# Kernel optimization log

Hardware: AMD Instinct MI355X
Metric: run time of the kernel (lower is better)

The kernel has to match this reference:

```python
import jax, jax.numpy as jnp
import numpy as np

EPS = 1e-5
NUM_GROUPS = 8


def setup_inputs() -> dict:
    key = jax.random.key(0)
    ks = jax.random.split(key, 7)
    B, C, D, H, W = 2, 128, 16, 16, 16
    s = 1.0 / np.sqrt(C)
    return {
        "x": jax.random.normal(ks[0], (B, C, D, H, W), dtype=jnp.float32),
        "Wq": jax.random.normal(ks[1], (C, C), dtype=jnp.float32) * s,
        "Wk": jax.random.normal(ks[2], (C, C), dtype=jnp.float32) * s,
        "Wv": jax.random.normal(ks[3], (C, C), dtype=jnp.float32) * s,
        "Wo": jax.random.normal(ks[4], (C, C), dtype=jnp.float32) * s,
        "gamma": jnp.ones((C,), dtype=jnp.float32),
        "beta": jnp.zeros((C,), dtype=jnp.float32),
    }


def reference(x, Wq, Wk, Wv, Wo, gamma, beta):
    B, C = x.shape[0], x.shape[1]
    spatial = x.shape[2:]
    xf = x.reshape(B, C, -1)  # [B, C, N]

    # 1x1 conv == channel-mixing matmul
    q = jnp.einsum('oc,bcn->bon', Wq, xf)
    k = jnp.einsum('oc,bcn->bon', Wk, xf)
    v = jnp.einsum('oc,bcn->bon', Wv, xf)

    # unscaled attention: qk[b,n,m] = sum_c q[b,c,n] k[b,c,m]
    w = jax.nn.softmax(jnp.einsum('bcn,bcm->bnm', q, k), axis=-1)  # [B, N, N]
    # h = v @ w^T : h[b,c,n] = sum_m v[b,c,m] w[b,n,m]
    h = jnp.einsum('bcm,bnm->bcn', v, w)
    h = jnp.einsum('oc,bcn->bon', Wo, h)

    y = xf + h
    # GroupNorm(8, C) over (C//G, N) per group
    g = y.reshape(B, NUM_GROUPS, C // NUM_GROUPS, -1)
    mu = jnp.mean(g, axis=(2, 3), keepdims=True)
    var = jnp.mean(jnp.square(g - mu), axis=(2, 3), keepdims=True)
    gn = ((g - mu) * jax.lax.rsqrt(var + EPS)).reshape(B, C, -1)
    out = gn * gamma[None, :, None] + beta[None, :, None]
    out = out * jax.nn.sigmoid(out)  # SiLU
    return out.reshape(B, C, *spatial)
```

## Files before the change

### kernel.cpp

```cpp
#include <hip/hip_runtime.h>

#define CC 128
#define NN 4096
#define NB 2
#define NSPLIT 8
#define TK 64
#define ITERS 8

typedef unsigned short ushort;
typedef unsigned int uint;
typedef __attribute__((ext_vector_type(8))) _Float16 h8;
typedef __attribute__((ext_vector_type(8))) short s8;
typedef __attribute__((ext_vector_type(4))) float f4;
#define MFMA16(a, b, c) __builtin_amdgcn_mfma_f32_16x16x32_f16(a, b, c, 0, 0, 0)
#define MFMAB(a, b, c)  __builtin_amdgcn_mfma_f32_16x16x32_bf16(a, b, c, 0, 0, 0)

__device__ __forceinline__ ushort f2h(float f) {
  _Float16 h = (_Float16)f;
  return *(ushort*)&h;
}
__device__ __forceinline__ ushort f2bf(float f) {
  uint u = __float_as_uint(f);
  u += 0x7fffu + ((u >> 16) & 1u);
  return (ushort)(u >> 16);
}
__device__ __forceinline__ float bf2f(ushort u) {
  return __uint_as_float((uint)u << 16);
}

__global__ __launch_bounds__(256) void qkv_mm(
    const float* __restrict__ x, const float* __restrict__ Wq,
    const float* __restrict__ Wk, const float* __restrict__ Wv,
    ushort* __restrict__ qT, ushort* __restrict__ kT, ushort* __restrict__ vB,
    float* __restrict__ stats) {
  __shared__ ushort Wh[CC][136];
  __shared__ ushort xs[32][136];
  const int t = threadIdx.x;
  const int n0 = blockIdx.x * 32;
  const int b = blockIdx.y;
  const int which = blockIdx.z;

  if (blockIdx.x == 0 && b == 0 && which == 0 && t < 32) stats[t] = 0.f;

  {
    int c0 = (t & 31) * 4;
    int n4 = (t >> 5) * 4;
    float4 r0 = *(const float4*)&x[((size_t)b * CC + c0 + 0) * NN + n0 + n4];
    float4 r1 = *(const float4*)&x[((size_t)b * CC + c0 + 1) * NN + n0 + n4];
    float4 r2 = *(const float4*)&x[((size_t)b * CC + c0 + 2) * NN + n0 + n4];
    float4 r3 = *(const float4*)&x[((size_t)b * CC + c0 + 3) * NN + n0 + n4];
    ushort4 w0, w1, w2, w3;
    w0.x = f2h(r0.x); w0.y = f2h(r1.x); w0.z = f2h(r2.x); w0.w = f2h(r3.x);
    w1.x = f2h(r0.y); w1.y = f2h(r1.y); w1.z = f2h(r2.y); w1.w = f2h(r3.y);
    w2.x = f2h(r0.z); w2.y = f2h(r1.z); w2.z = f2h(r2.z); w2.w = f2h(r3.z);
    w3.x = f2h(r0.w); w3.y = f2h(r1.w); w3.z = f2h(r2.w); w3.w = f2h(r3.w);
    *(ushort4*)&xs[n4 + 0][c0] = w0;
    *(ushort4*)&xs[n4 + 1][c0] = w1;
    *(ushort4*)&xs[n4 + 2][c0] = w2;
    *(ushort4*)&xs[n4 + 3][c0] = w3;
  }

  {
    const float* W = (which == 0) ? Wq : (which == 1) ? Wk : Wv;
#pragma unroll
    for (int i = 0; i < 16; ++i) {
      int slot = t + 256 * i;
      int o = slot >> 5, c4 = (slot & 31) * 4;
      float4 w4 = *(const float4*)&W[o * CC + c4];
      ushort4 p; p.x = f2h(w4.x); p.y = f2h(w4.y); p.z = f2h(w4.z); p.w = f2h(w4.w);
      *(ushort4*)&Wh[o][c4] = p;
    }
  }
  __syncthreads();

  const int wv = t >> 6, lane = t & 63;
  const int quad = lane >> 4, l16 = lane & 15;

  if (which < 2) {
    ushort* out = which ? kT : qT;
    f4 acc[2][2];
#pragma unroll
    for (int ot = 0; ot < 2; ++ot)
#pragma unroll
      for (int nt = 0; nt < 2; ++nt) acc[ot][nt] = (f4){0.f, 0.f, 0.f, 0.f};
#pragma unroll
    for (int kk = 0; kk < 4; ++kk) {
      h8 a0 = *(const h8*)&Wh[(wv * 2 + 0) * 16 + l16][kk * 32 + quad * 8];
      h8 a1 = *(const h8*)&Wh[(wv * 2 + 1) * 16 + l16][kk * 32 + quad * 8];
#pragma unroll
      for (int nt = 0; nt < 2; ++nt) {
        h8 bb = *(const h8*)&xs[nt * 16 + l16][kk * 32 + quad * 8];
        acc[0][nt] = MFMA16(a0, bb, acc[0][nt]);
        acc[1][nt] = MFMA16(a1, bb, acc[1][nt]);
      }
    }
#pragma unroll
    for (int ot = 0; ot < 2; ++ot)
#pragma unroll
      for (int nt = 0; nt < 2; ++nt) {
        f4 a = acc[ot][nt];
        ushort4 p; p.x = f2h(a[0]); p.y = f2h(a[1]); p.z = f2h(a[2]); p.w = f2h(a[3]);
        *(ushort4*)&out[((size_t)b * NN + n0 + nt * 16 + l16) * CC +
                        (wv * 2 + ot) * 16 + quad * 4] = p;
      }
  } else {
    f4 acc[2][2];
#pragma unroll
    for (int ci = 0; ci < 2; ++ci)
#pragma unroll
      for (int nt = 0; nt < 2; ++nt) acc[ci][nt] = (f4){0.f, 0.f, 0.f, 0.f};
#pragma unroll
    for (int kk = 0; kk < 4; ++kk) {
      h8 a0 = *(const h8*)&xs[0 * 16 + l16][kk * 32 + quad * 8];
      h8 a1 = *(const h8*)&xs[1 * 16 + l16][kk * 32 + quad * 8];
      h8 b0 = *(const h8*)&Wh[(wv * 2 + 0) * 16 + l16][kk * 32 + quad * 8];
      h8 b1 = *(const h8*)&Wh[(wv * 2 + 1) * 16 + l16][kk * 32 + quad * 8];
      acc[0][0] = MFMA16(a0, b0, acc[0][0]);
      acc[0][1] = MFMA16(a1, b0, acc[0][1]);
      acc[1][0] = MFMA16(a0, b1, acc[1][0]);
      acc[1][1] = MFMA16(a1, b1, acc[1][1]);
    }
#pragma unroll
    for (int ci = 0; ci < 2; ++ci)
#pragma unroll
      for (int nt = 0; nt < 2; ++nt) {
        f4 a = acc[ci][nt];
        ushort4 p; p.x = f2bf(a[0]); p.y = f2bf(a[1]); p.z = f2bf(a[2]); p.w = f2bf(a[3]);
        *(ushort4*)&vB[((size_t)b * CC + (wv * 2 + ci) * 16 + l16) * NN +
                       n0 + nt * 16 + quad * 4] = p;
      }
  }
}

__global__ __launch_bounds__(256) void attn_split(
    const ushort* __restrict__ qTg, const ushort* __restrict__ kTg,
    const ushort* __restrict__ vBg, ushort* __restrict__ Op,
    float* __restrict__ Lg) {
  __shared__ ushort ksT[TK][136];
  __shared__ ushort vs[CC][72];
  __shared__ ushort psb[4][32][72];

  const int t = threadIdx.x;
  const int b = blockIdx.z;
  const int split = blockIdx.y;
  const int n0 = blockIdx.x * 128;
  const int wv = t >> 6;
  const int lane = t & 63;
  const int quad = lane >> 4;
  const int l16 = lane & 15;
  const int nw = n0 + wv * 32;
  const int m00 = split * (NN / NSPLIT);

  const int krow = t >> 4, kcol = (t & 15) * 8;
  const int vrow = t >> 3, vcol = (t & 7) * 8;
  const ushort* kbp = kTg + ((size_t)b * NN + m00 + krow) * CC + kcol;
  const ushort* vbp = vBg + ((size_t)b * CC + vrow) * NN + m00 + vcol;

  const size_t qb0 = ((size_t)b * NN + nw + l16) * CC + quad * 8;
  const size_t qb1 = qb0 + (size_t)16 * CC;
  h8 aq[2][4];
#pragma unroll
  for (int kk = 0; kk < 4; ++kk) {
    aq[0][kk] = *(const h8*)&qTg[qb0 + kk * 32];
    aq[1][kk] = *(const h8*)&qTg[qb1 + kk * 32];
  }

  int4 k0 = *(const int4*)&kbp[0];
  int4 k1 = *(const int4*)&kbp[16 * CC];
  int4 k2 = *(const int4*)&kbp[32 * CC];
  int4 k3 = *(const int4*)&kbp[48 * CC];
  int4 v0 = *(const int4*)&vbp[0];
  int4 v1 = *(const int4*)&vbp[(size_t)32 * NN];
  int4 v2 = *(const int4*)&vbp[(size_t)64 * NN];
  int4 v3 = *(const int4*)&vbp[(size_t)96 * NN];

  s8 ones;
#pragma unroll
  for (int i = 0; i < 8; ++i) ones[i] = (short)0x3F80;

  f4 o[2][8];
#pragma unroll
  for (int j = 0; j < 2; ++j)
#pragma unroll
    for (int ct = 0; ct < 8; ++ct) o[j][ct] = (f4){0.f, 0.f, 0.f, 0.f};
  f4 oL[2];
  oL[0] = (f4){0.f, 0.f, 0.f, 0.f};
  oL[1] = (f4){0.f, 0.f, 0.f, 0.f};

  for (int kt = 0; kt < ITERS; ++kt) {
    *(int4*)&ksT[krow][kcol]      = k0;
    *(int4*)&ksT[krow + 16][kcol] = k1;
    *(int4*)&ksT[krow + 32][kcol] = k2;
    *(int4*)&ksT[krow + 48][kcol] = k3;
    *(int4*)&vs[vrow][vcol]       = v0;
    *(int4*)&vs[vrow + 32][vcol]  = v1;
    *(int4*)&vs[vrow + 64][vcol]  = v2;
    *(int4*)&vs[vrow + 96][vcol]  = v3;
    __syncthreads();

    {
      int ktn = (kt + 1 < ITERS) ? kt + 1 : kt;
      const ushort* kp = kbp + (size_t)ktn * TK * CC;
      const ushort* vp = vbp + (size_t)ktn * TK;
      k0 = *(const int4*)&kp[0];
      k1 = *(const int4*)&kp[16 * CC];
      k2 = *(const int4*)&kp[32 * CC];
      k3 = *(const int4*)&kp[48 * CC];
      v0 = *(const int4*)&vp[0];
      v1 = *(const int4*)&vp[(size_t)32 * NN];
      v2 = *(const int4*)&vp[(size_t)64 * NN];
      v3 = *(const int4*)&vp[(size_t)96 * NN];
    }

    f4 s[2][4];
#pragma unroll
    for (int j = 0; j < 2; ++j)
#pragma unroll
      for (int mt = 0; mt < 4; ++mt) s[j][mt] = (f4){0.f, 0.f, 0.f, 0.f};
#pragma unroll
    for (int kk = 0; kk < 4; ++kk) {
      h8 b0 = *(const h8*)&ksT[ 0 + l16][kk * 32 + quad * 8];
      h8 b1 = *(const h8*)&ksT[16 + l16][kk * 32 + quad * 8];
      h8 b2 = *(const h8*)&ksT[32 + l16][kk * 32 + quad * 8];
      h8 b3 = *(const h8*)&ksT[48 + l16][kk * 32 + quad * 8];
#pragma unroll
      for (int j = 0; j < 2; ++j) {
        s[j][0] = MFMA16(b0, aq[j][kk], s[j][0]);
        s[j][1] = MFMA16(b1, aq[j][kk], s[j][1]);
        s[j][2] = MFMA16(b2, aq[j][kk], s[j][2]);
        s[j][3] = MFMA16(b3, aq[j][kk], s[j][3]);
      }
    }

#pragma unroll
    for (int j = 0; j < 2; ++j)
#pragma unroll
      for (int mt = 0; mt < 4; ++mt) {
        ushort4 pk;
        pk.x = f2bf(__expf(s[j][mt][0]));
        pk.y = f2bf(__expf(s[j][mt][1]));
        pk.z = f2bf(__expf(s[j][mt][2]));
        pk.w = f2bf(__expf(s[j][mt][3]));
        *(ushort4*)&psb[wv][j * 16 + l16][mt * 16 + quad * 4] = pk;
      }

#pragma unroll
    for (int mk = 0; mk < 2; ++mk) {
      s8 bp0 = *(const s8*)&psb[wv][ 0 + l16][mk * 32 + quad * 8];
      s8 bp1 = *(const s8*)&psb[wv][16 + l16][mk * 32 + quad * 8];
#pragma unroll
      for (int ct = 0; ct < 8; ++ct) {
        s8 a = *(const s8*)&vs[ct * 16 + l16][mk * 32 + quad * 8];
        o[0][ct] = MFMAB(a, bp0, o[0][ct]);
        o[1][ct] = MFMAB(a, bp1, o[1][ct]);
      }
      oL[0] = MFMAB(ones, bp0, oL[0]);
      oL[1] = MFMAB(ones, bp1, oL[1]);
    }
    __syncthreads();
  }

#pragma unroll
  for (int j = 0; j < 2; ++j) {
    if (quad == 0)
      Lg[((size_t)(split * NB + b)) * NN + nw + j * 16 + l16] = oL[j][0];
    size_t nb_ = ((size_t)(split * NB + b) * NN + nw + j * 16 + l16) * CC + quad * 4;
    ushort4 p;
#pragma unroll
    for (int ct = 0; ct < 8; ++ct) {
      f4 a = o[j][ct];
      p.x = f2bf(a[0]); p.y = f2bf(a[1]); p.z = f2bf(a[2]); p.w = f2bf(a[3]);
      *(ushort4*)&Op[nb_ + ct * 16] = p;
    }
  }
}

__global__ __launch_bounds__(256) void proj_mm(
    const float* __restrict__ x, const float* __restrict__ Wo,
    const ushort* __restrict__ Op, const float* __restrict__ Lg,
    float* __restrict__ y, float* __restrict__ stats) {
  __shared__ ushort Wh[CC][136];
  __shared__ ushort hT[32][136];
  __shared__ float Linv[32];
  const int t = threadIdx.x;
  const int n0 = blockIdx.x * 32;
  const int b = blockIdx.y;

#pragma unroll
  for (int i = 0; i < 16; ++i) {
    int slot = t + 256 * i;
    int o = slot >> 5, c4 = (slot & 31) * 4;
    float4 w4 = *(const float4*)&Wo[o * CC + c4];
    ushort4 p; p.x = f2h(w4.x); p.y = f2h(w4.y); p.z = f2h(w4.z); p.w = f2h(w4.w);
    *(ushort4*)&Wh[o][c4] = p;
  }
  if (t < 32) {
    float l = 0.f;
#pragma unroll
    for (int s = 0; s < NSPLIT; ++s)
      l += Lg[(size_t)(s * NB + b) * NN + n0 + t];
    Linv[t] = 1.f / l;
  }
  __syncthreads();

#pragma unroll
  for (int i = 0; i < 16; ++i) {
    int slot = t + 256 * i;
    int n = slot >> 5, c4 = (slot & 31) * 4;
    size_t base = ((size_t)(n0 + n)) * CC + c4;
    float a0 = 0.f, a1 = 0.f, a2 = 0.f, a3 = 0.f;
#pragma unroll
    for (int s = 0; s < NSPLIT; ++s) {
      ushort4 u = *(const ushort4*)&Op[(size_t)(s * NB + b) * NN * CC + base];
      a0 += bf2f(u.x); a1 += bf2f(u.y); a2 += bf2f(u.z); a3 += bf2f(u.w);
    }
    float li = Linv[n];
    ushort4 p;
    p.x = f2h(a0 * li); p.y = f2h(a1 * li);
    p.z = f2h(a2 * li); p.w = f2h(a3 * li);
    *(ushort4*)&hT[n][c4] = p;
  }
  __syncthreads();

  const int wv = t >> 6, lane = t & 63;
  const int quad = lane >> 4, l16 = lane & 15;

  f4 acc[2][2];
#pragma unroll
  for (int nt = 0; nt < 2; ++nt)
#pragma unroll
    for (int ot = 0; ot < 2; ++ot) acc[nt][ot] = (f4){0.f, 0.f, 0.f, 0.f};
#pragma unroll
  for (int kk = 0; kk < 4; ++kk) {
    h8 a0 = *(const h8*)&hT[0 * 16 + l16][kk * 32 + quad * 8];
    h8 a1 = *(const h8*)&hT[1 * 16 + l16][kk * 32 + quad * 8];
    h8 b0 = *(const h8*)&Wh[(wv * 2 + 0) * 16 + l16][kk * 32 + quad * 8];
    h8 b1 = *(const h8*)&Wh[(wv * 2 + 1) * 16 + l16][kk * 32 + quad * 8];
    acc[0][0] = MFMA16(a0, b0, acc[0][0]);
    acc[0][1] = MFMA16(a0, b1, acc[0][1]);
    acc[1][0] = MFMA16(a1, b0, acc[1][0]);
    acc[1][1] = MFMA16(a1, b1, acc[1][1]);
  }

#pragma unroll
  for (int ot = 0; ot < 2; ++ot) {
    const int o = (wv * 2 + ot) * 16 + l16;
    const int g = wv * 2 + ot;
    float s = 0.f, sq = 0.f;
#pragma unroll
    for (int nt = 0; nt < 2; ++nt) {
      size_t addr = ((size_t)b * CC + o) * NN + n0 + nt * 16 + quad * 4;
      float4 xv = *(const float4*)&x[addr];
      f4 a = acc[nt][ot];
      float4 yy;
      yy.x = a[0] + xv.x; yy.y = a[1] + xv.y;
      yy.z = a[2] + xv.z; yy.w = a[3] + xv.w;
      *(float4*)&y[addr] = yy;
      s += yy.x + yy.y + yy.z + yy.w;
      sq += yy.x * yy.x + yy.y * yy.y + yy.z * yy.z + yy.w * yy.w;
    }
#pragma unroll
    for (int off = 1; off < 64; off <<= 1) {
      s += __shfl_xor(s, off);
      sq += __shfl_xor(sq, off);
    }
    if (lane == 0) {
      atomicAdd(&stats[(b * 8 + g) * 2 + 0], s);
      atomicAdd(&stats[(b * 8 + g) * 2 + 1], sq);
    }
  }
}

__global__ __launch_bounds__(256) void gn_silu(
    const float* __restrict__ y, const float* __restrict__ stats,
    const float* __restrict__ gamma, const float* __restrict__ beta,
    float* __restrict__ out) {
  const int tid = blockIdx.x * 256 + threadIdx.x;
  const int i4 = tid * 4;
  const int c = (i4 >> 12) & (CC - 1);
  const int b = i4 >> 19;
  const int g = c >> 4;
  const float inv = 1.f / 65536.f;
  float sum = stats[(b * 8 + g) * 2 + 0];
  float sq  = stats[(b * 8 + g) * 2 + 1];
  float mean = sum * inv;
  float var = sq * inv - mean * mean;
  float rs = rsqrtf(var + 1e-5f);
  float ga = gamma[c], be = beta[c];
  float4 v4 = *(const float4*)&y[i4];
  float4 r;
  float o;
  o = (v4.x - mean) * rs * ga + be; r.x = o / (1.f + __expf(-o));
  o = (v4.y - mean) * rs * ga + be; r.y = o / (1.f + __expf(-o));
  o = (v4.z - mean) * rs * ga + be; r.z = o / (1.f + __expf(-o));
  o = (v4.w - mean) * rs * ga + be; r.w = o / (1.f + __expf(-o));
  *(float4*)&out[i4] = r;
}

extern "C" void kernel_launch(void* const* d_in, const int* in_sizes, int n_in,
                              void* d_out, int out_size, void* d_ws, size_t ws_size,
                              hipStream_t stream) {
  const float* x     = (const float*)d_in[0];
  const float* Wq    = (const float*)d_in[1];
  const float* Wk    = (const float*)d_in[2];
  const float* Wv    = (const float*)d_in[3];
  const float* Wo    = (const float*)d_in[4];
  const float* gamma = (const float*)d_in[5];
  const float* beta  = (const float*)d_in[6];
  float* out = (float*)d_out;
  float* ws  = (float*)d_ws;

  const size_t M = (size_t)NB * CC * NN;
  ushort* Op = (ushort*)ws;
  ushort* qT = (ushort*)ws + (size_t)NSPLIT * M;
  ushort* kT = qT + M;
  ushort* vB = kT + M;
  float* y = (float*)(vB + M);
  float* Lg = y + M;
  float* stats = Lg + (size_t)NSPLIT * NB * NN;

  qkv_mm<<<dim3(NN / 32, NB, 3), 256, 0, stream>>>(x, Wq, Wk, Wv, qT, kT, vB, stats);
  attn_split<<<dim3(NN / 128, NSPLIT, NB), 256, 0, stream>>>(qT, kT, vB, Op, Lg);
  proj_mm<<<dim3(NN / 32, NB), 256, 0, stream>>>(x, Wo, Op, Lg, y, stats);
  gn_silu<<<dim3((int)(M / 1024)), 256, 0, stream>>>(y, stats, gamma, beta, out);
}
```

Before: 144.9 us.

## Fuse GroupNorm+SiLU into projection kernel via grid-wide atomic barrier

Removes the separate gn_silu kernel and the fp32 y intermediate buffer. The projection kernel keeps its residual-added outputs in registers, waits at a software grid barrier (an atomic counter spun on by one thread per block) until every block has added its GroupNorm statistics, then normalizes, applies SiLU and writes the output directly. This saves one launch plus a full write and read of y, but relies on all 256 blocks being resident at the same time. Otherwise the spin-wait deadlocks.

```diff
diff --git a/kernel.cpp b/kernel.cpp
--- a/kernel.cpp
+++ b/kernel.cpp
@@ -6,6 +6,7 @@
 #define NSPLIT 8
 #define TK 64
 #define ITERS 8
+#define NPROJ (NN / 32 * NB)
 
 typedef unsigned short ushort;
 typedef unsigned int uint;
@@ -40,7 +41,7 @@
   const int b = blockIdx.y;
   const int which = blockIdx.z;
 
-  if (blockIdx.x == 0 && b == 0 && which == 0 && t < 32) stats[t] = 0.f;
+  if (blockIdx.x == 0 && b == 0 && which == 0 && t < 40) stats[t] = 0.f;
 
   {
     int c0 = (t & 31) * 4;
@@ -278,13 +279,16 @@
 __global__ __launch_bounds__(256) void proj_mm(
     const float* __restrict__ x, const float* __restrict__ Wo,
     const ushort* __restrict__ Op, const float* __restrict__ Lg,
-    float* __restrict__ y, float* __restrict__ stats) {
+    const float* __restrict__ gamma, const float* __restrict__ beta,
+    float* __restrict__ out, float* __restrict__ stats) {
   __shared__ ushort Wh[CC][136];
   __shared__ ushort hT[32][136];
   __shared__ float Linv[32];
+  __shared__ float sstat[32];
   const int t = threadIdx.x;
   const int n0 = blockIdx.x * 32;
   const int b = blockIdx.y;
+  uint* done = (uint*)(stats + 32);
 
 #pragma unroll
   for (int i = 0; i < 16; ++i) {
@@ -342,6 +346,7 @@
     acc[1][1] = MFMA16(a1, b1, acc[1][1]);
   }
 
+  f4 yy[2][2];
 #pragma unroll
   for (int ot = 0; ot < 2; ++ot) {
     const int o = (wv * 2 + ot) * 16 + l16;
@@ -352,12 +357,11 @@
       size_t addr = ((size_t)b * CC + o) * NN + n0 + nt * 16 + quad * 4;
       float4 xv = *(const float4*)&x[addr];
       f4 a = acc[nt][ot];
-      float4 yy;
-      yy.x = a[0] + xv.x; yy.y = a[1] + xv.y;
-      yy.z = a[2] + xv.z; yy.w = a[3] + xv.w;
-      *(float4*)&y[addr] = yy;
-      s += yy.x + yy.y + yy.z + yy.w;
-      sq += yy.x * yy.x + yy.y * yy.y + yy.z * yy.z + yy.w * yy.w;
+      yy[ot][nt][0] = a[0] + xv.x; yy[ot][nt][1] = a[1] + xv.y;
+      yy[ot][nt][2] = a[2] + xv.z; yy[ot][nt][3] = a[3] + xv.w;
+      s += yy[ot][nt][0] + yy[ot][nt][1] + yy[ot][nt][2] + yy[ot][nt][3];
+      sq += yy[ot][nt][0] * yy[ot][nt][0] + yy[ot][nt][1] * yy[ot][nt][1] +
+            yy[ot][nt][2] * yy[ot][nt][2] + yy[ot][nt][3] * yy[ot][nt][3];
     }
 #pragma unroll
     for (int off = 1; off < 64; off <<= 1) {
@@ -369,32 +373,42 @@
       atomicAdd(&stats[(b * 8 + g) * 2 + 1], sq);
     }
   }
-}
-
-__global__ __launch_bounds__(256) void gn_silu(
-    const float* __restrict__ y, const float* __restrict__ stats,
-    const float* __restrict__ gamma, const float* __restrict__ beta,
-    float* __restrict__ out) {
-  const int tid = blockIdx.x * 256 + threadIdx.x;
-  const int i4 = tid * 4;
-  const int c = (i4 >> 12) & (CC - 1);
-  const int b = i4 >> 19;
-  const int g = c >> 4;
+
+  __syncthreads();
+  if (t == 0) {
+    __hip_atomic_fetch_add(done, 1u, __ATOMIC_ACQ_REL, __HIP_MEMORY_SCOPE_AGENT);
+    while (__hip_atomic_load(done, __ATOMIC_ACQUIRE, __HIP_MEMORY_SCOPE_AGENT) <
+           (uint)NPROJ) {
+      __builtin_amdgcn_s_sleep(8);
+    }
+  }
+  __syncthreads();
+  if (t < 32)
+    sstat[t] = __hip_atomic_load(&stats[t], __ATOMIC_ACQUIRE,
+                                 __HIP_MEMORY_SCOPE_AGENT);
+  __syncthreads();
+
   const float inv = 1.f / 65536.f;
-  float sum = stats[(b * 8 + g) * 2 + 0];
-  float sq  = stats[(b * 8 + g) * 2 + 1];
-  float mean = sum * inv;
-  float var = sq * inv - mean * mean;
-  float rs = rsqrtf(var + 1e-5f);
-  float ga = gamma[c], be = beta[c];
-  float4 v4 = *(const float4*)&y[i4];
-  float4 r;
-  float o;
-  o = (v4.x - mean) * rs * ga + be; r.x = o / (1.f + __expf(-o));
-  o = (v4.y - mean) * rs * ga + be; r.y = o / (1.f + __expf(-o));
-  o = (v4.z - mean) * rs * ga + be; r.z = o / (1.f + __expf(-o));
-  o = (v4.w - mean) * rs * ga + be; r.w = o / (1.f + __expf(-o));
-  *(float4*)&out[i4] = r;
+#pragma unroll
+  for (int ot = 0; ot < 2; ++ot) {
+    const int o = (wv * 2 + ot) * 16 + l16;
+    const int g = wv * 2 + ot;
+    float mean = sstat[(b * 8 + g) * 2 + 0] * inv;
+    float var = sstat[(b * 8 + g) * 2 + 1] * inv - mean * mean;
+    float rs = rsqrtf(var + 1e-5f);
+    float ga = gamma[o], be = beta[o];
+#pragma unroll
+    for (int nt = 0; nt < 2; ++nt) {
+      size_t addr = ((size_t)b * CC + o) * NN + n0 + nt * 16 + quad * 4;
+      float4 r;
+      float v;
+      v = (yy[ot][nt][0] - mean) * rs * ga + be; r.x = v / (1.f + __expf(-v));
+      v = (yy[ot][nt][1] - mean) * rs * ga + be; r.y = v / (1.f + __expf(-v));
+      v = (yy[ot][nt][2] - mean) * rs * ga + be; r.z = v / (1.f + __expf(-v));
+      v = (yy[ot][nt][3] - mean) * rs * ga + be; r.w = v / (1.f + __expf(-v));
+      *(float4*)&out[addr] = r;
+    }
+  }
 }
 
 extern "C" void kernel_launch(void* const* d_in, const int* in_sizes, int n_in,
@@ -415,12 +429,11 @@
   ushort* qT = (ushort*)ws + (size_t)NSPLIT * M;
   ushort* kT = qT + M;
   ushort* vB = kT + M;
-  float* y = (float*)(vB + M);
-  float* Lg = y + M;
+  float* Lg = (float*)(vB + M);
   float* stats = Lg + (size_t)NSPLIT * NB * NN;
 
   qkv_mm<<<dim3(NN / 32, NB, 3), 256, 0, stream>>>(x, Wq, Wk, Wv, qT, kT, vB, stats);
   attn_split<<<dim3(NN / 128, NSPLIT, NB), 256, 0, stream>>>(qT, kT, vB, Op, Lg);
-  proj_mm<<<dim3(NN / 32, NB), 256, 0, stream>>>(x, Wo, Op, Lg, y, stats);
-  gn_silu<<<dim3((int)(M / 1024)), 256, 0, stream>>>(y, stats, gamma, beta, out);
-}
+  proj_mm<<<dim3(NN / 32, NB), 256, 0, stream>>>(x, Wo, Op, Lg, gamma, beta, out,
+                                                 stats);
+}
```

New measurement: 154.5 us. 6.7% more time.
